# Optimization experiments

Measured on AMD Instinct MI355X. Metric: run time of the kernel, lower is better.

The kernel has to match this reference:

```python
import jax, jax.numpy as jnp
import numpy as np
import math

B, T, D, H = 64, 512, 512, 512


def setup_inputs() -> dict:
    key = jax.random.key(0)
    ks = jax.random.split(key, 32)
    stdv = 1.0 / math.sqrt(H)  # matches reset_parameters()
    u = lambda k, shape: jax.random.uniform(k, shape, jnp.float32, -stdv, stdv)
    inp = {
        "x": jax.random.normal(ks[0], (B, T, D), jnp.float32),
        "h0": jax.random.normal(ks[1], (B, H), jnp.float32),
        "ctx": jax.random.normal(ks[2], (B, T, H), jnp.float32),
    }
    # 9 Linear layers (torch convention: y = x @ W.T + b), weights AND biases uniform(-stdv, stdv)
    names_shapes = [
        ("W_ir", (H, D)), ("b_ir", (H,)), ("W_hr", (H, H)), ("b_hr", (H,)), ("W_pr", (H, H)), ("b_pr", (H,)),
        ("W_ii", (H, D)), ("b_ii", (H,)), ("W_hi", (H, H)), ("b_hi", (H,)), ("W_pi", (H, H)), ("b_pi", (H,)),
        ("W_in", (H, D)), ("b_in", (H,)), ("W_hn", (H, H)), ("b_hn", (H,)), ("W_pn", (H, H)), ("b_pn", (H,)),
    ]
    for i, (nm, sh) in enumerate(names_shapes):
        inp[nm] = u(ks[3 + i], sh)
    return inp


def _forward(x, h0, ctx, W_ir, b_ir, W_hr, b_hr, W_pr, b_pr,
             W_ii, b_ii, W_hi, b_hi, W_pi, b_pi,
             W_in, b_in, W_hn, b_hn, W_pn, b_pn):
    # Precompute all hidden-independent projections for every step: [T,B,H]
    xr = jnp.einsum('btd,hd->tbh', x, W_ir) + b_ir
    xi = jnp.einsum('btd,hd->tbh', x, W_ii) + b_ii
    xn = jnp.einsum('btd,hd->tbh', x, W_in) + b_in
    pr = jnp.einsum('bte,he->tbh', ctx, W_pr) + b_pr
    pi = jnp.einsum('bte,he->tbh', ctx, W_pi) + b_pi
    pn = jnp.einsum('bte,he->tbh', ctx, W_pn) + b_pn

    def step(h, inputs_t):
        xr_t, xi_t, xn_t, pr_t, pi_t, pn_t = inputs_t
        r = jax.nn.sigmoid(xr_t + h @ W_hr.T + b_hr + pr_t)
        i = jax.nn.sigmoid(xi_t + h @ W_hi.T + b_hi + pi_t)
        n = jnp.tanh(xn_t + (r * h) @ W_hn.T + b_hn + pn_t)
        hy = (1.0 - i) * h + i * n
        return hy, hy

    hT, ys = jax.lax.scan(step, h0, (xr, xi, xn, pr, pi, pn))
    return ys.transpose(1, 0, 2), hT  # output [B,T,H], final hidden [B,H]


def reference(x, h0, ctx, W_ir, b_ir, W_hr, b_hr, W_pr, b_pr,
              W_ii, b_ii, W_hi, b_hi, W_pi, b_pi,
              W_in, b_in, W_hn, b_hn, W_pn, b_pn):
    return _forward(x, h0, ctx, W_ir, b_ir, W_hr, b_hr, W_pr, b_pr,
                    W_ii, b_ii, W_hi, b_hi, W_pi, b_pi,
                    W_in, b_in, W_hn, b_hn, W_pn, b_pn)
```

## Files before the change

kernel.cpp:

```cpp
#include <hip/hip_runtime.h>
#include <hip/hip_bf16.h>

typedef __attribute__((ext_vector_type(8))) short short8;
typedef __attribute__((ext_vector_type(4))) float floatx4;

#define TBH ((size_t)16777216)

__device__ __forceinline__ float bfbits2f(unsigned short b) {
  return __uint_as_float(((unsigned int)b) << 16);
}
__device__ __forceinline__ unsigned short f2bf(float f) {
  unsigned int u = __float_as_uint(f);
  unsigned int r = (u + 0x7fffu + ((u >> 16) & 1u)) >> 16;
  return (unsigned short)r;
}

__device__ __forceinline__ void dev_store(unsigned int* p, unsigned int v) {
  __hip_atomic_store(p, v, __ATOMIC_RELAXED, __HIP_MEMORY_SCOPE_AGENT);
}
__device__ __forceinline__ unsigned int dev_load(const unsigned int* p) {
  return __hip_atomic_load(p, __ATOMIC_RELAXED, __HIP_MEMORY_SCOPE_AGENT);
}

#define LBAR()                                              \
  do {                                                      \
    asm volatile("s_waitcnt lgkmcnt(0)" ::: "memory");      \
    __builtin_amdgcn_s_barrier();                           \
    __builtin_amdgcn_sched_barrier(0);                      \
  } while (0)

__global__ void prep_kernel(const float* __restrict__ h0,
                            unsigned int* __restrict__ hpub,
                            unsigned int* __restrict__ rhpub,
                            const float* __restrict__ Whr,
                            const float* __restrict__ Whi,
                            const float* __restrict__ Whn,
                            unsigned short* __restrict__ Whb) {
  int i = blockIdx.x * 256 + threadIdx.x;
  if (i < 64 * 512) {
    hpub[i] = ((unsigned int)f2bf(h0[i])) << 16;
    rhpub[i] = 0u;
  }
#pragma unroll
  for (int rep = 0; rep < 3; ++rep) {
    int j = i + rep * 262144;
    float v = (j < 262144) ? Whr[j] : ((j < 524288) ? Whi[j - 262144] : Whn[j - 524288]);
    Whb[j] = f2bf(v);
  }
}

struct PreArgs {
  const float* x;
  const float* ctx;
  const float* Wi[3];
  const float* Wp[3];
  const float* bi[3];
  const float* bh[3];
  const float* bp[3];
  unsigned short* G;
};

__global__ __launch_bounds__(256) void gemm_pre(PreArgs args) {
  __shared__ short8 a_sm[512];
  __shared__ short8 b_sm[512];
  const int tid = threadIdx.x;
  const int gate = blockIdx.z;
  const int n0 = blockIdx.x * 128;
  const int m0 = blockIdx.y * 128;
  const int wave = tid >> 6, lane = tid & 63;
  const int wm = (wave & 1) * 64, wn = (wave >> 1) * 64;
  const int lm = lane & 15, lq = lane >> 4;
  const float* Wi = args.Wi[gate];
  const float* Wp = args.Wp[gate];

  floatx4 acc[4][4];
#pragma unroll
  for (int i = 0; i < 4; ++i)
#pragma unroll
    for (int j = 0; j < 4; ++j) acc[i][j] = floatx4{0.f, 0.f, 0.f, 0.f};

  for (int kb = 0; kb < 32; ++kb) {
    const float* asrc = (kb < 16) ? args.x : args.ctx;
    const float* bsrc = (kb < 16) ? Wi : Wp;
    const int k0 = (kb & 15) * 32;
    __syncthreads();
#pragma unroll
    for (int c = 0; c < 2; ++c) {
      int s = c * 256 + tid;
      int row = s >> 2, sub = s & 3;
      const float* ap = asrc + (size_t)(m0 + row) * 512 + k0 + sub * 8;
      const float* bp = bsrc + (size_t)(n0 + row) * 512 + k0 + sub * 8;
      float4 a0 = *(const float4*)ap, a1 = *(const float4*)(ap + 4);
      float4 b0 = *(const float4*)bp, b1 = *(const float4*)(bp + 4);
      short8 av, bv;
      av[0] = (short)f2bf(a0.x); av[1] = (short)f2bf(a0.y);
      av[2] = (short)f2bf(a0.z); av[3] = (short)f2bf(a0.w);
      av[4] = (short)f2bf(a1.x); av[5] = (short)f2bf(a1.y);
      av[6] = (short)f2bf(a1.z); av[7] = (short)f2bf(a1.w);
      bv[0] = (short)f2bf(b0.x); bv[1] = (short)f2bf(b0.y);
      bv[2] = (short)f2bf(b0.z); bv[3] = (short)f2bf(b0.w);
      bv[4] = (short)f2bf(b1.x); bv[5] = (short)f2bf(b1.y);
      bv[6] = (short)f2bf(b1.z); bv[7] = (short)f2bf(b1.w);
      a_sm[row * 4 + sub] = av;
      b_sm[row * 4 + sub] = bv;
    }
    __syncthreads();
    short8 af[4], bf[4];
#pragma unroll
    for (int i = 0; i < 4; ++i) af[i] = a_sm[(wm + i * 16 + lm) * 4 + lq];
#pragma unroll
    for (int j = 0; j < 4; ++j) bf[j] = b_sm[(wn + j * 16 + lm) * 4 + lq];
#pragma unroll
    for (int i = 0; i < 4; ++i)
#pragma unroll
      for (int j = 0; j < 4; ++j)
        acc[i][j] = __builtin_amdgcn_mfma_f32_16x16x32_bf16(af[i], bf[j], acc[i][j], 0, 0, 0);
  }

#pragma unroll
  for (int j = 0; j < 4; ++j) {
    int n = n0 + wn + j * 16 + lm;
    float bias = args.bi[gate][n] + args.bh[gate][n] + args.bp[gate][n];
#pragma unroll
    for (int i = 0; i < 4; ++i) {
      int mbase = m0 + wm + i * 16 + lq * 4;
#pragma unroll
      for (int r = 0; r < 4; ++r) {
        int m = mbase + r;
        int t = m & 511, b = m >> 9;
        args.G[(size_t)gate * TBH + (size_t)(t * 64 + b) * 512 + n] = f2bf(acc[i][j][r] + bias);
      }
    }
  }
}

__global__ __launch_bounds__(512, 2) void recur_kernel(
    const unsigned short* __restrict__ G,
    const unsigned short* __restrict__ Whb,
    const float* __restrict__ h0,
    unsigned int* __restrict__ hpub,
    unsigned int* __restrict__ rhpub,
    float* __restrict__ ys,
    float* __restrict__ hT) {
  __shared__ short8 fragbuf[1024];

  const int tid = threadIdx.x;
  const int g = blockIdx.x >> 2;
  const int cb = blockIdx.x & 3;
  const int b0 = g * 16;
  const int c0 = cb * 128;
  const int wave = tid >> 6, lane = tid & 63;
  const int lm = lane & 15, lq = lane >> 4;
  const int cw0 = c0 + wave * 16;
  const int prow = lq * 4;

  short8 wrl[4], wil[4], wnl[4];
  short8 wrr[12], wir[12], wnr[12];
  {
    const unsigned short* Wb = Whb + (size_t)(cw0 + lm) * 512 + lq * 8;
#pragma unroll
    for (int q = 0; q < 4; ++q) {
      const int kb = cb * 4 + q;
      wrl[q] = *(const short8*)(Wb + 0 * 262144 + kb * 32);
      wil[q] = *(const short8*)(Wb + 1 * 262144 + kb * 32);
      wnl[q] = *(const short8*)(Wb + 2 * 262144 + kb * 32);
    }
#pragma unroll
    for (int j = 0; j < 12; ++j) {
      const int kb = (((cb + 1 + (j >> 2)) & 3) << 2) + (j & 3);
      wrr[j] = *(const short8*)(Wb + 0 * 262144 + kb * 32);
      wir[j] = *(const short8*)(Wb + 1 * 262144 + kb * 32);
      wnr[j] = *(const short8*)(Wb + 2 * 262144 + kb * 32);
    }
  }

  const int srow = tid >> 5;
  const int skk = (tid * 4) & 127;
  const int sl = srow + 16 * ((skk >> 3) & 3);
  const int su2 = ((skk >> 5) * 64 + sl) * 2 + ((skk >> 2) & 1);
  uint2* f2 = (uint2*)fragbuf;
  unsigned short* fus = (unsigned short*)fragbuf;

  const int kcol = cw0 + lm;
  const int eidx = ((kcol >> 5) * 64 + 16 * ((kcol >> 3) & 3)) * 8 + (kcol & 7);

  float hreg[4], ireg[4];
#pragma unroll
  for (int r = 0; r < 4; ++r) hreg[r] = h0[(size_t)(b0 + prow + r) * 512 + kcol];
  {
    const float* hp = h0 + (size_t)(b0 + srow) * 512 + c0 + skk;
    float4 v = *(const float4*)hp;
    uint2 p;
    p.x = (unsigned int)f2bf(v.x) | ((unsigned int)f2bf(v.y) << 16);
    p.y = (unsigned int)f2bf(v.z) | ((unsigned int)f2bf(v.w) << 16);
    f2[su2 + cb * 512] = p;
  }
  __syncthreads();

  for (int t = 0; t < 512; ++t) {
    const unsigned int tgh = (unsigned int)t;
    const unsigned int tgr = (unsigned int)(t + 1);

    float gr[4], gi[4];
    const unsigned short* Gt = G + ((size_t)(t * 64 + b0 + prow)) * 512 + kcol;
#pragma unroll
    for (int r = 0; r < 4; ++r) {
      gr[r] = bfbits2f(Gt[r * 512]);
      gi[r] = bfbits2f(Gt[TBH + r * 512]);
    }

    floatx4 ar = {0.f, 0.f, 0.f, 0.f}, ai = {0.f, 0.f, 0.f, 0.f};
    {
      unsigned int v[12];
      unsigned int* hb = hpub + (unsigned)(b0 + srow) * 512;
#pragma unroll
      for (int s = 0; s < 3; ++s) {
        const int off = (((cb + 1 + s) & 3) << 7) + skk;
#pragma unroll
        for (int j = 0; j < 4; ++j) v[s * 4 + j] = dev_load(hb + off + j);
      }
#pragma unroll
      for (int q = 0; q < 4; ++q) {
        short8 hf = fragbuf[(cb * 4 + q) * 64 + lane];
        ar = __builtin_amdgcn_mfma_f32_16x16x32_bf16(hf, wrl[q], ar, 0, 0, 0);
        ai = __builtin_amdgcn_mfma_f32_16x16x32_bf16(hf, wil[q], ai, 0, 0, 0);
      }
      for (;;) {
        bool ok = true;
#pragma unroll
        for (int i = 0; i < 12; ++i) ok &= ((v[i] & 0xffffu) == tgh);
        if (ok) break;
#pragma unroll
        for (int s = 0; s < 3; ++s) {
          bool st = false;
#pragma unroll
          for (int j = 0; j < 4; ++j) st |= ((v[s * 4 + j] & 0xffffu) != tgh);
          if (st) {
            const int off = (((cb + 1 + s) & 3) << 7) + skk;
#pragma unroll
            for (int j = 0; j < 4; ++j) v[s * 4 + j] = dev_load(hb + off + j);
          }
        }
      }
#pragma unroll
      for (int s = 0; s < 3; ++s) {
        const int rcb = (cb + 1 + s) & 3;
        uint2 p;
        p.x = (v[s * 4 + 0] >> 16) | (v[s * 4 + 1] & 0xffff0000u);
        p.y = (v[s * 4 + 2] >> 16) | (v[s * 4 + 3] & 0xffff0000u);
        f2[su2 + rcb * 512] = p;
      }
    }
    LBAR();

#pragma unroll
    for (int j = 0; j < 12; ++j) {
      const int kb = (((cb + 1 + (j >> 2)) & 3) << 2) + (j & 3);
      short8 hf = fragbuf[kb * 64 + lane];
      ar = __builtin_amdgcn_mfma_f32_16x16x32_bf16(hf, wrr[j], ar, 0, 0, 0);
      ai = __builtin_amdgcn_mfma_f32_16x16x32_bf16(hf, wir[j], ai, 0, 0, 0);
    }

    {
      unsigned int* rb = rhpub + (unsigned)(b0 + prow) * 512 + kcol;
#pragma unroll
      for (int r = 0; r < 4; ++r) {
        float sv = 1.f / (1.f + __expf(-(ar[r] + gr[r])));
        float rh = sv * hreg[r];
        ireg[r] = 1.f / (1.f + __expf(-(ai[r] + gi[r])));
        unsigned short rbits = f2bf(rh);
        dev_store(rb + r * 512, (((unsigned int)rbits) << 16) | tgr);
        fus[eidx + (prow + r) * 8] = rbits;
      }
    }
    LBAR();

    float gn[4];
#pragma unroll
    for (int r = 0; r < 4; ++r) gn[r] = bfbits2f(Gt[2 * TBH + r * 512]);

    floatx4 an = {0.f, 0.f, 0.f, 0.f};
    {
      unsigned int v[12];
      unsigned int* rbb = rhpub + (unsigned)(b0 + srow) * 512;
#pragma unroll
      for (int s = 0; s < 3; ++s) {
        const int off = (((cb + 1 + s) & 3) << 7) + skk;
#pragma unroll
        for (int j = 0; j < 4; ++j) v[s * 4 + j] = dev_load(rbb + off + j);
      }
#pragma unroll
      for (int q = 0; q < 4; ++q) {
        short8 hf = fragbuf[(cb * 4 + q) * 64 + lane];
        an = __builtin_amdgcn_mfma_f32_16x16x32_bf16(hf, wnl[q], an, 0, 0, 0);
      }
      for (;;) {
        bool ok = true;
#pragma unroll
        for (int i = 0; i < 12; ++i) ok &= ((v[i] & 0xffffu) == tgr);
        if (ok) break;
#pragma unroll
        for (int s = 0; s < 3; ++s) {
          bool st = false;
#pragma unroll
          for (int j = 0; j < 4; ++j) st |= ((v[s * 4 + j] & 0xffffu) != tgr);
          if (st) {
            const int off = (((cb + 1 + s) & 3) << 7) + skk;
#pragma unroll
            for (int j = 0; j < 4; ++j) v[s * 4 + j] = dev_load(rbb + off + j);
          }
        }
      }
#pragma unroll
      for (int s = 0; s < 3; ++s) {
        const int rcb = (cb + 1 + s) & 3;
        uint2 p;
        p.x = (v[s * 4 + 0] >> 16) | (v[s * 4 + 1] & 0xffff0000u);
        p.y = (v[s * 4 + 2] >> 16) | (v[s * 4 + 3] & 0xffff0000u);
        f2[su2 + rcb * 512] = p;
      }
    }
    LBAR();

#pragma unroll
    for (int j = 0; j < 12; ++j) {
      const int kb = (((cb + 1 + (j >> 2)) & 3) << 2) + (j & 3);
      short8 hf = fragbuf[kb * 64 + lane];
      an = __builtin_amdgcn_mfma_f32_16x16x32_bf16(hf, wnr[j], an, 0, 0, 0);
    }

    {
      unsigned int* hb = hpub + (unsigned)(b0 + prow) * 512 + kcol;
      float* yp = ys + (size_t)(b0 + prow) * 262144 + (size_t)t * 512 + kcol;
#pragma unroll
      for (int r = 0; r < 4; ++r) {
        float pre = an[r] + gn[r];
        float e = __expf(2.f * pre);
        float nv = 1.f - 2.f / (e + 1.f);
        float hy = (1.f - ireg[r]) * hreg[r] + ireg[r] * nv;
        hreg[r] = hy;
        unsigned short hbits = f2bf(hy);
        dev_store(hb + r * 512, (((unsigned int)hbits) << 16) | tgr);
        yp[(size_t)r * 262144] = hy;
        fus[eidx + (prow + r) * 8] = hbits;
      }
      if (t == 511) {
#pragma unroll
        for (int r = 0; r < 4; ++r) hT[(size_t)(b0 + prow + r) * 512 + kcol] = hreg[r];
      }
    }
    LBAR();
  }
}

extern "C" void kernel_launch(void* const* d_in, const int* in_sizes, int n_in,
                              void* d_out, int out_size, void* d_ws, size_t ws_size,
                              hipStream_t stream) {
  typedef const float* cfp;
  cfp x = (cfp)d_in[0];
  cfp h0 = (cfp)d_in[1];
  cfp ctx = (cfp)d_in[2];

  PreArgs pa;
  pa.x = x;
  pa.ctx = ctx;
  for (int gi = 0; gi < 3; ++gi) {
    pa.Wi[gi] = (cfp)d_in[3 + 6 * gi];
    pa.bi[gi] = (cfp)d_in[4 + 6 * gi];
    pa.bh[gi] = (cfp)d_in[6 + 6 * gi];
    pa.Wp[gi] = (cfp)d_in[7 + 6 * gi];
    pa.bp[gi] = (cfp)d_in[8 + 6 * gi];
  }
  cfp Whr = (cfp)d_in[5], Whi = (cfp)d_in[11], Whn = (cfp)d_in[17];

  char* ws = (char*)d_ws;
  unsigned short* G = (unsigned short*)ws;
  size_t off = (size_t)3 * TBH * 2;
  unsigned short* Whb = (unsigned short*)(ws + off);
  off += (size_t)3 * 262144 * 2;
  unsigned int* hpub = (unsigned int*)(ws + off);
  off += (size_t)64 * 512 * 4;
  unsigned int* rhpub = (unsigned int*)(ws + off);
  off += (size_t)64 * 512 * 4;
  pa.G = G;

  float* out = (float*)d_out;
  float* ys = out;
  float* hT = out + (size_t)64 * 512 * 512;

  prep_kernel<<<1024, 256, 0, stream>>>(h0, hpub, rhpub, Whr, Whi, Whn, Whb);
  dim3 gp(4, 256, 3);
  gemm_pre<<<gp, 256, 0, stream>>>(pa);
  recur_kernel<<<16, 512, 0, stream>>>(G, Whb, h0, hpub, rhpub, ys, hT);
}
```

Baseline: 4.173 ms.

## Replace r*h grid sync with partial-sum exchange of r-gate products

The recurrent kernel drops the second cross-block handshake, which published r*h. Each block now computes partial r-gate products over its own K slice for all 64 output columns of its wave and publishes them through a tagged, double-buffered buffer. Peers then reduce those partial sums locally, so r*h for the local columns is built in LDS without a second full h-exchange round. The i-gate weights move to LDS and the n-gate weights stay in registers, G loads are prefetched one step ahead, and h publication is double-buffered. In exchange each step loads and stores more global data (48 partial-sum loads per thread), and the float partial sums lose their low two mantissa bits to the tag.

```diff
diff --git a/kernel.cpp b/kernel.cpp
--- a/kernel.cpp
+++ b/kernel.cpp
@@ -31,7 +31,7 @@
 
 __global__ void prep_kernel(const float* __restrict__ h0,
                             unsigned int* __restrict__ hpub,
-                            unsigned int* __restrict__ rhpub,
+                            unsigned int* __restrict__ PrB,
                             const float* __restrict__ Whr,
                             const float* __restrict__ Whi,
                             const float* __restrict__ Whn,
@@ -39,8 +39,9 @@
   int i = blockIdx.x * 256 + threadIdx.x;
   if (i < 64 * 512) {
     hpub[i] = ((unsigned int)f2bf(h0[i])) << 16;
-    rhpub[i] = 0u;
-  }
+    hpub[32768 + i] = 0x8000u;
+  }
+  PrB[i] = 0u;
 #pragma unroll
   for (int rep = 0; rep < 3; ++rep) {
     int j = i + rep * 262144;
@@ -139,10 +140,11 @@
     const unsigned short* __restrict__ Whb,
     const float* __restrict__ h0,
     unsigned int* __restrict__ hpub,
-    unsigned int* __restrict__ rhpub,
+    unsigned int* __restrict__ PrB,
     float* __restrict__ ys,
     float* __restrict__ hT) {
   __shared__ short8 fragbuf[1024];
+  __shared__ short8 iwsm[8192];
 
   const int tid = threadIdx.x;
   const int g = blockIdx.x >> 2;
@@ -151,28 +153,26 @@
   const int c0 = cb * 128;
   const int wave = tid >> 6, lane = tid & 63;
   const int lm = lane & 15, lq = lane >> 4;
-  const int cw0 = c0 + wave * 16;
+  const int w64 = wave * 64;
+  const int kcol = c0 + wave * 16 + lm;
   const int prow = lq * 4;
 
-  short8 wrl[4], wil[4], wnl[4];
-  short8 wrr[12], wir[12], wnr[12];
-  {
-    const unsigned short* Wb = Whb + (size_t)(cw0 + lm) * 512 + lq * 8;
-#pragma unroll
-    for (int q = 0; q < 4; ++q) {
-      const int kb = cb * 4 + q;
-      wrl[q] = *(const short8*)(Wb + 0 * 262144 + kb * 32);
-      wil[q] = *(const short8*)(Wb + 1 * 262144 + kb * 32);
-      wnl[q] = *(const short8*)(Wb + 2 * 262144 + kb * 32);
-    }
-#pragma unroll
-    for (int j = 0; j < 12; ++j) {
-      const int kb = (((cb + 1 + (j >> 2)) & 3) << 2) + (j & 3);
-      wrr[j] = *(const short8*)(Wb + 0 * 262144 + kb * 32);
-      wir[j] = *(const short8*)(Wb + 1 * 262144 + kb * 32);
-      wnr[j] = *(const short8*)(Wb + 2 * 262144 + kb * 32);
-    }
-  }
+  for (int s = tid; s < 8192; s += 512) {
+    int wv = s >> 10, kb = (s >> 6) & 15, l = s & 63;
+    iwsm[s] = *(const short8*)(Whb + 262144 +
+        (size_t)(c0 + (wv << 4) + (l & 15)) * 512 + kb * 32 + (l >> 4) * 8);
+  }
+  short8 wpr[4][4], wnw[16];
+#pragma unroll
+  for (int n = 0; n < 4; ++n)
+#pragma unroll
+    for (int q = 0; q < 4; ++q)
+      wpr[n][q] = *(const short8*)(Whb +
+          (size_t)(w64 + n * 16 + lm) * 512 + (cb * 4 + q) * 32 + lq * 8);
+#pragma unroll
+  for (int kb = 0; kb < 16; ++kb)
+    wnw[kb] = *(const short8*)(Whb + 2 * 262144 +
+        (size_t)kcol * 512 + kb * 32 + lq * 8);
 
   const int srow = tid >> 5;
   const int skk = (tid * 4) & 127;
@@ -181,174 +181,186 @@
   uint2* f2 = (uint2*)fragbuf;
   unsigned short* fus = (unsigned short*)fragbuf;
 
-  const int kcol = cw0 + lm;
-  const int eidx = ((kcol >> 5) * 64 + 16 * ((kcol >> 3) & 3)) * 8 + (kcol & 7);
-
-  float hreg[4], ireg[4];
-#pragma unroll
-  for (int r = 0; r < 4; ++r) hreg[r] = h0[(size_t)(b0 + prow + r) * 512 + kcol];
-  {
-    const float* hp = h0 + (size_t)(b0 + srow) * 512 + c0 + skk;
-    float4 v = *(const float4*)hp;
-    uint2 p;
-    p.x = (unsigned int)f2bf(v.x) | ((unsigned int)f2bf(v.y) << 16);
-    p.y = (unsigned int)f2bf(v.z) | ((unsigned int)f2bf(v.w) << 16);
-    f2[su2 + cb * 512] = p;
-  }
+  int pub[4], ppos[16], pfix[16];
+#pragma unroll
+  for (int r = 0; r < 4; ++r) pub[r] = (b0 + prow + r) * 512 + kcol;
+#pragma unroll
+  for (int n = 0; n < 4; ++n)
+#pragma unroll
+    for (int r = 0; r < 4; ++r) {
+      int col = w64 + n * 16 + lm;
+      ppos[n * 4 + r] = (prow + r) * 512 + col;
+      pfix[n * 4 + r] = (col >> 5) * 512 + ((col >> 3) & 3) * 128 + (col & 7) + (prow + r) * 8;
+    }
+  const int ecol = (kcol >> 5) * 512 + ((kcol >> 3) & 3) * 128 + (kcol & 7);
+  const int groff = b0 * 512;
+
+  float hreg[4];
+#pragma unroll
+  for (int r = 0; r < 4; ++r) hreg[r] = h0[pub[r]];
+#pragma unroll
+  for (int r = 0; r < 4; ++r) fus[ecol + (prow + r) * 8] = f2bf(hreg[r]);
   __syncthreads();
 
+  unsigned short grc[16], gic[4], gnc[4];
+#pragma unroll
+  for (int k = 0; k < 16; ++k) grc[k] = G[(size_t)(groff + ppos[k])];
+#pragma unroll
+  for (int r = 0; r < 4; ++r) {
+    gic[r] = G[TBH + (size_t)pub[r]];
+    gnc[r] = G[2 * TBH + (size_t)pub[r]];
+  }
+
   for (int t = 0; t < 512; ++t) {
-    const unsigned int tgh = (unsigned int)t;
-    const unsigned int tgr = (unsigned int)(t + 1);
-
-    float gr[4], gi[4];
-    const unsigned short* Gt = G + ((size_t)(t * 64 + b0 + prow)) * 512 + kcol;
-#pragma unroll
-    for (int r = 0; r < 4; ++r) {
-      gr[r] = bfbits2f(Gt[r * 512]);
-      gi[r] = bfbits2f(Gt[TBH + r * 512]);
-    }
-
-    floatx4 ar = {0.f, 0.f, 0.f, 0.f}, ai = {0.f, 0.f, 0.f, 0.f};
-    {
-      unsigned int v[12];
-      unsigned int* hb = hpub + (unsigned)(b0 + srow) * 512;
+    const unsigned int htag = (unsigned int)t;
+    const unsigned int prtag = (unsigned int)((t + 1) & 3);
+    const unsigned int* hsrc = hpub + (t & 1) * 32768;
+    unsigned int* prdst = PrB + (size_t)(t & 1) * 131072 + g * 32768 + cb * 8192;
+    const unsigned int* prsrc = PrB + (size_t)(t & 1) * 131072 + g * 32768;
+
+    floatx4 pr[4];
+#pragma unroll
+    for (int n = 0; n < 4; ++n) pr[n] = floatx4{0.f, 0.f, 0.f, 0.f};
+    short8 hfq[4];
+#pragma unroll
+    for (int q = 0; q < 4; ++q) hfq[q] = fragbuf[(cb * 4 + q) * 64 + lane];
+#pragma unroll
+    for (int n = 0; n < 4; ++n)
+#pragma unroll
+      for (int q = 0; q < 4; ++q)
+        pr[n] = __builtin_amdgcn_mfma_f32_16x16x32_bf16(hfq[q], wpr[n][q], pr[n], 0, 0, 0);
+#pragma unroll
+    for (int n = 0; n < 4; ++n)
+#pragma unroll
+      for (int r = 0; r < 4; ++r)
+        dev_store((unsigned int*)prdst + ppos[n * 4 + r],
+                  (__float_as_uint(pr[n][r]) & 0xFFFFFFFCu) | prtag);
+
+    unsigned int hv[12];
+    const unsigned int* hb = hsrc + (unsigned)(b0 + srow) * 512;
+#pragma unroll
+    for (int s = 0; s < 3; ++s) {
+      const int off = (((cb + 1 + s) & 3) << 7) + skk;
+#pragma unroll
+      for (int j = 0; j < 4; ++j) hv[s * 4 + j] = dev_load(hb + off + j);
+    }
+    unsigned int pv[48];
+#pragma unroll
+    for (int s = 0; s < 3; ++s) {
+      const int sb = ((cb + 1 + s) & 3) * 8192;
+#pragma unroll
+      for (int k = 0; k < 16; ++k) pv[s * 16 + k] = dev_load(prsrc + sb + ppos[k]);
+    }
+
+    for (;;) {
+      bool ok = true;
+#pragma unroll
+      for (int i = 0; i < 12; ++i) ok &= ((hv[i] & 0xffffu) == htag);
+      if (ok) break;
 #pragma unroll
       for (int s = 0; s < 3; ++s) {
-        const int off = (((cb + 1 + s) & 3) << 7) + skk;
-#pragma unroll
-        for (int j = 0; j < 4; ++j) v[s * 4 + j] = dev_load(hb + off + j);
-      }
-#pragma unroll
-      for (int q = 0; q < 4; ++q) {
-        short8 hf = fragbuf[(cb * 4 + q) * 64 + lane];
-        ar = __builtin_amdgcn_mfma_f32_16x16x32_bf16(hf, wrl[q], ar, 0, 0, 0);
-        ai = __builtin_amdgcn_mfma_f32_16x16x32_bf16(hf, wil[q], ai, 0, 0, 0);
-      }
-      for (;;) {
-        bool ok = true;
-#pragma unroll
-        for (int i = 0; i < 12; ++i) ok &= ((v[i] & 0xffffu) == tgh);
-        if (ok) break;
-#pragma unroll
-        for (int s = 0; s < 3; ++s) {
-          bool st = false;
-#pragma unroll
-          for (int j = 0; j < 4; ++j) st |= ((v[s * 4 + j] & 0xffffu) != tgh);
-          if (st) {
-            const int off = (((cb + 1 + s) & 3) << 7) + skk;
-#pragma unroll
-            for (int j = 0; j < 4; ++j) v[s * 4 + j] = dev_load(hb + off + j);
-          }
+        bool st = false;
+#pragma unroll
+        for (int j = 0; j < 4; ++j) st |= ((hv[s * 4 + j] & 0xffffu) != htag);
+        if (st) {
+          const int off = (((cb + 1 + s) & 3) << 7) + skk;
+#pragma unroll
+          for (int j = 0; j < 4; ++j) hv[s * 4 + j] = dev_load(hb + off + j);
         }
       }
+    }
+#pragma unroll
+    for (int s = 0; s < 3; ++s) {
+      const int rcb = (cb + 1 + s) & 3;
+      uint2 p;
+      p.x = (hv[s * 4 + 0] >> 16) | (hv[s * 4 + 1] & 0xffff0000u);
+      p.y = (hv[s * 4 + 2] >> 16) | (hv[s * 4 + 3] & 0xffff0000u);
+      f2[su2 + rcb * 512] = p;
+    }
+    LBAR();
+
+    floatx4 ia = {0.f, 0.f, 0.f, 0.f};
+#pragma unroll
+    for (int kb = 0; kb < 16; ++kb)
+      ia = __builtin_amdgcn_mfma_f32_16x16x32_bf16(
+          fragbuf[kb * 64 + lane], iwsm[(wave * 16 + kb) * 64 + lane], ia, 0, 0, 0);
+
+    for (;;) {
+      bool ok = true;
+#pragma unroll
+      for (int i = 0; i < 48; ++i) ok &= ((pv[i] & 3u) == prtag);
+      if (ok) break;
 #pragma unroll
       for (int s = 0; s < 3; ++s) {
-        const int rcb = (cb + 1 + s) & 3;
-        uint2 p;
-        p.x = (v[s * 4 + 0] >> 16) | (v[s * 4 + 1] & 0xffff0000u);
-        p.y = (v[s * 4 + 2] >> 16) | (v[s * 4 + 3] & 0xffff0000u);
-        f2[su2 + rcb * 512] = p;
-      }
-    }
-    LBAR();
-
-#pragma unroll
-    for (int j = 0; j < 12; ++j) {
-      const int kb = (((cb + 1 + (j >> 2)) & 3) << 2) + (j & 3);
-      short8 hf = fragbuf[kb * 64 + lane];
-      ar = __builtin_amdgcn_mfma_f32_16x16x32_bf16(hf, wrr[j], ar, 0, 0, 0);
-      ai = __builtin_amdgcn_mfma_f32_16x16x32_bf16(hf, wir[j], ai, 0, 0, 0);
-    }
-
-    {
-      unsigned int* rb = rhpub + (unsigned)(b0 + prow) * 512 + kcol;
-#pragma unroll
-      for (int r = 0; r < 4; ++r) {
-        float sv = 1.f / (1.f + __expf(-(ar[r] + gr[r])));
-        float rh = sv * hreg[r];
-        ireg[r] = 1.f / (1.f + __expf(-(ai[r] + gi[r])));
-        unsigned short rbits = f2bf(rh);
-        dev_store(rb + r * 512, (((unsigned int)rbits) << 16) | tgr);
-        fus[eidx + (prow + r) * 8] = rbits;
-      }
-    }
-    LBAR();
-
-    float gn[4];
-#pragma unroll
-    for (int r = 0; r < 4; ++r) gn[r] = bfbits2f(Gt[2 * TBH + r * 512]);
-
-    floatx4 an = {0.f, 0.f, 0.f, 0.f};
-    {
-      unsigned int v[12];
-      unsigned int* rbb = rhpub + (unsigned)(b0 + srow) * 512;
-#pragma unroll
-      for (int s = 0; s < 3; ++s) {
-        const int off = (((cb + 1 + s) & 3) << 7) + skk;
-#pragma unroll
-        for (int j = 0; j < 4; ++j) v[s * 4 + j] = dev_load(rbb + off + j);
-      }
-#pragma unroll
-      for (int q = 0; q < 4; ++q) {
-        short8 hf = fragbuf[(cb * 4 + q) * 64 + lane];
-        an = __builtin_amdgcn_mfma_f32_16x16x32_bf16(hf, wnl[q], an, 0, 0, 0);
-      }
-      for (;;) {
-        bool ok = true;
-#pragma unroll
-        for (int i = 0; i < 12; ++i) ok &= ((v[i] & 0xffffu) == tgr);
-        if (ok) break;
-#pragma unroll
-        for (int s = 0; s < 3; ++s) {
-          bool st = false;
-#pragma unroll
-          for (int j = 0; j < 4; ++j) st |= ((v[s * 4 + j] & 0xffffu) != tgr);
-          if (st) {
-            const int off = (((cb + 1 + s) & 3) << 7) + skk;
-#pragma unroll
-            for (int j = 0; j < 4; ++j) v[s * 4 + j] = dev_load(rbb + off + j);
-          }
+        bool st = false;
+#pragma unroll
+        for (int k = 0; k < 16; ++k) st |= ((pv[s * 16 + k] & 3u) != prtag);
+        if (st) {
+          const int sb = ((cb + 1 + s) & 3) * 8192;
+#pragma unroll
+          for (int k = 0; k < 16; ++k) pv[s * 16 + k] = dev_load(prsrc + sb + ppos[k]);
         }
       }
-#pragma unroll
-      for (int s = 0; s < 3; ++s) {
-        const int rcb = (cb + 1 + s) & 3;
-        uint2 p;
-        p.x = (v[s * 4 + 0] >> 16) | (v[s * 4 + 1] & 0xffff0000u);
-        p.y = (v[s * 4 + 2] >> 16) | (v[s * 4 + 3] & 0xffff0000u);
-        f2[su2 + rcb * 512] = p;
-      }
-    }
+    }
+
+    unsigned short rhb[16];
+#pragma unroll
+    for (int k = 0; k < 16; ++k) {
+      int n = k >> 2, r = k & 3;
+      float rsum = pr[n][r] + bfbits2f(grc[k]) +
+                   __uint_as_float(pv[k] & 0xFFFFFFFCu) +
+                   __uint_as_float(pv[16 + k] & 0xFFFFFFFCu) +
+                   __uint_as_float(pv[32 + k] & 0xFFFFFFFCu);
+      float rv = 1.f / (1.f + __expf(-rsum));
+      rhb[k] = f2bf(rv * bfbits2f(fus[pfix[k]]));
+    }
+    float ireg[4];
+#pragma unroll
+    for (int r = 0; r < 4; ++r) ireg[r] = 1.f / (1.f + __expf(-(ia[r] + bfbits2f(gic[r]))));
     LBAR();
 
 #pragma unroll
-    for (int j = 0; j < 12; ++j) {
-      const int kb = (((cb + 1 + (j >> 2)) & 3) << 2) + (j & 3);
-      short8 hf = fragbuf[kb * 64 + lane];
-      an = __builtin_amdgcn_mfma_f32_16x16x32_bf16(hf, wnr[j], an, 0, 0, 0);
-    }
-
-    {
-      unsigned int* hb = hpub + (unsigned)(b0 + prow) * 512 + kcol;
-      float* yp = ys + (size_t)(b0 + prow) * 262144 + (size_t)t * 512 + kcol;
-#pragma unroll
-      for (int r = 0; r < 4; ++r) {
-        float pre = an[r] + gn[r];
-        float e = __expf(2.f * pre);
-        float nv = 1.f - 2.f / (e + 1.f);
-        float hy = (1.f - ireg[r]) * hreg[r] + ireg[r] * nv;
-        hreg[r] = hy;
-        unsigned short hbits = f2bf(hy);
-        dev_store(hb + r * 512, (((unsigned int)hbits) << 16) | tgr);
-        yp[(size_t)r * 262144] = hy;
-        fus[eidx + (prow + r) * 8] = hbits;
-      }
-      if (t == 511) {
-#pragma unroll
-        for (int r = 0; r < 4; ++r) hT[(size_t)(b0 + prow + r) * 512 + kcol] = hreg[r];
-      }
-    }
+    for (int k = 0; k < 16; ++k) fus[pfix[k]] = rhb[k];
+    LBAR();
+
+    floatx4 na = {0.f, 0.f, 0.f, 0.f};
+#pragma unroll
+    for (int kb = 0; kb < 16; ++kb)
+      na = __builtin_amdgcn_mfma_f32_16x16x32_bf16(
+          fragbuf[kb * 64 + lane], wnw[kb], na, 0, 0, 0);
+
+    const int tp = (t + 1 < 512) ? t + 1 : 511;
+    unsigned short grn[16], gin[4], gnn[4];
+#pragma unroll
+    for (int k = 0; k < 16; ++k) grn[k] = G[(size_t)tp * 32768 + groff + ppos[k]];
+#pragma unroll
+    for (int r = 0; r < 4; ++r) {
+      gin[r] = G[TBH + (size_t)tp * 32768 + pub[r]];
+      gnn[r] = G[2 * TBH + (size_t)tp * 32768 + pub[r]];
+    }
+    LBAR();
+
+    unsigned int* hdst = hpub + ((t + 1) & 1) * 32768;
+#pragma unroll
+    for (int r = 0; r < 4; ++r) {
+      float pre = na[r] + bfbits2f(gnc[r]);
+      float e = __expf(2.f * pre);
+      float nv = 1.f - 2.f / (e + 1.f);
+      float hy = (1.f - ireg[r]) * hreg[r] + ireg[r] * nv;
+      hreg[r] = hy;
+      unsigned short hbits = f2bf(hy);
+      dev_store(hdst + pub[r], (((unsigned int)hbits) << 16) | (unsigned int)(t + 1));
+      fus[ecol + (prow + r) * 8] = hbits;
+      ys[(size_t)(b0 + prow + r) * 262144 + (size_t)t * 512 + kcol] = hy;
+    }
+    if (t == 511) {
+#pragma unroll
+      for (int r = 0; r < 4; ++r) hT[pub[r]] = hreg[r];
+    }
+#pragma unroll
+    for (int k = 0; k < 16; ++k) grc[k] = grn[k];
+#pragma unroll
+    for (int r = 0; r < 4; ++r) { gic[r] = gin[r]; gnc[r] = gnn[r]; }
     LBAR();
   }
 }
@@ -379,17 +391,17 @@
   unsigned short* Whb = (unsigned short*)(ws + off);
   off += (size_t)3 * 262144 * 2;
   unsigned int* hpub = (unsigned int*)(ws + off);
-  off += (size_t)64 * 512 * 4;
-  unsigned int* rhpub = (unsigned int*)(ws + off);
-  off += (size_t)64 * 512 * 4;
+  off += (size_t)2 * 64 * 512 * 4;
+  unsigned int* PrB = (unsigned int*)(ws + off);
+  off += (size_t)2 * 4 * 4 * 16 * 512 * 4;
   pa.G = G;
 
   float* out = (float*)d_out;
   float* ys = out;
   float* hT = out + (size_t)64 * 512 * 512;
 
-  prep_kernel<<<1024, 256, 0, stream>>>(h0, hpub, rhpub, Whr, Whi, Whn, Whb);
+  prep_kernel<<<1024, 256, 0, stream>>>(h0, hpub, PrB, Whr, Whi, Whn, Whb);
   dim3 gp(4, 256, 3);
   gemm_pre<<<gp, 256, 0, stream>>>(pa);
-  recur_kernel<<<16, 512, 0, stream>>>(G, Whb, h0, hpub, rhpub, ys, hT);
-}
+  recur_kernel<<<16, 512, 0, stream>>>(G, Whb, h0, hpub, PrB, ys, hT);
+}
```

Result: slower. 10.76 ms (+157.8%).

## Split recurrence across 32 blocks with XCD-local fast sync path

Applied to the files above, without the earlier changes.

Launches 32 recurrent blocks instead of 16, each covering 8 batch rows instead of 16, so per-step work is spread over more CUs. At startup the blocks check whether all four column-partners share the same XCD and pass a ping test. If they do, the exchange uses L2-coherent sc0 vector loads and volatile stores instead of agent-scope atomics. It also prefetches the next step's G values and uses dwordx4 polling loads. The risk is that half the lanes idle (only lq<2 is active) and that the fast path relies on an XCD co-location assumption, which falls back to the slow path when it does not hold.

```diff
diff --git a/kernel.cpp b/kernel.cpp
--- a/kernel.cpp
+++ b/kernel.cpp
@@ -3,6 +3,7 @@
 
 typedef __attribute__((ext_vector_type(8))) short short8;
 typedef __attribute__((ext_vector_type(4))) float floatx4;
+typedef __attribute__((ext_vector_type(4))) unsigned int uintx4;
 
 #define TBH ((size_t)16777216)
 
@@ -20,6 +21,50 @@
 }
 __device__ __forceinline__ unsigned int dev_load(const unsigned int* p) {
   return __hip_atomic_load(p, __ATOMIC_RELAXED, __HIP_MEMORY_SCOPE_AGENT);
+}
+
+template <bool FAST>
+__device__ __forceinline__ void exst(unsigned int* p, unsigned int v) {
+  if constexpr (FAST) {
+    *(volatile unsigned int*)p = v;
+  } else {
+    dev_store(p, v);
+  }
+}
+
+template <bool FAST>
+__device__ __forceinline__ uintx4 exld4(const unsigned int* p) {
+  uintx4 r;
+  if constexpr (FAST) {
+    asm volatile("global_load_dwordx4 %0, %1, off sc0\n\ts_waitcnt vmcnt(0)"
+                 : "=&v"(r) : "v"(p) : "memory");
+  } else {
+    r[0] = dev_load(p); r[1] = dev_load(p + 1);
+    r[2] = dev_load(p + 2); r[3] = dev_load(p + 3);
+  }
+  return r;
+}
+
+template <bool FAST>
+__device__ __forceinline__ void exld4x3(const unsigned int* p0, const unsigned int* p1,
+                                        const unsigned int* p2,
+                                        uintx4& a, uintx4& b, uintx4& c) {
+  if constexpr (FAST) {
+    asm volatile(
+        "global_load_dwordx4 %0, %3, off sc0\n\t"
+        "global_load_dwordx4 %1, %4, off sc0\n\t"
+        "global_load_dwordx4 %2, %5, off sc0\n\t"
+        "s_waitcnt vmcnt(0)"
+        : "=&v"(a), "=&v"(b), "=&v"(c)
+        : "v"(p0), "v"(p1), "v"(p2) : "memory");
+  } else {
+    a = exld4<false>(p0); b = exld4<false>(p1); c = exld4<false>(p2);
+  }
+}
+
+__device__ __forceinline__ bool tagok(uintx4 v, unsigned int tag) {
+  return ((v[0] & 0xffffu) == tag) & ((v[1] & 0xffffu) == tag) &
+         ((v[2] & 0xffffu) == tag) & ((v[3] & 0xffffu) == tag);
 }
 
 #define LBAR()                                              \
@@ -32,6 +77,7 @@
 __global__ void prep_kernel(const float* __restrict__ h0,
                             unsigned int* __restrict__ hpub,
                             unsigned int* __restrict__ rhpub,
+                            unsigned int* __restrict__ aux,
                             const float* __restrict__ Whr,
                             const float* __restrict__ Whi,
                             const float* __restrict__ Whn,
@@ -41,6 +87,7 @@
     hpub[i] = ((unsigned int)f2bf(h0[i])) << 16;
     rhpub[i] = 0u;
   }
+  if (i < 576) aux[i] = 0u;
 #pragma unroll
   for (int rep = 0; rep < 3; ++rep) {
     int j = i + rep * 262144;
@@ -134,223 +181,272 @@
   }
 }
 
+template <bool FAST>
+__device__ __forceinline__ void recur_body(
+    const unsigned short* __restrict__ G,
+    const unsigned short* __restrict__ Whb,
+    const float* __restrict__ h0,
+    unsigned int* __restrict__ hpub,
+    unsigned int* __restrict__ rhpub,
+    float* __restrict__ ys,
+    float* __restrict__ hT,
+    short8* fragbuf) {
+  const int tid = threadIdx.x;
+  const int bid = blockIdx.x;
+  const int c = bid & 7;
+  const int cb = bid >> 3;
+  const int b0 = c * 8;
+  const int c0 = cb * 128;
+  const int wave = tid >> 6, lane = tid & 63;
+  const int lm = lane & 15, lq = lane >> 4;
+  const int kcol = c0 + wave * 16 + lm;
+  const int prow = lq * 4;
+  const bool pv = (lq < 2);
+
+  const unsigned short* Wb = Whb + (size_t)kcol * 512 + lq * 8;
+  short8 wrl[4], wil[4], wnl[4], wrr[12], wir[12], wnr[12];
+#pragma unroll
+  for (int q = 0; q < 4; ++q) {
+    const int kb = cb * 4 + q;
+    wrl[q] = *(const short8*)(Wb + 0 * 262144 + kb * 32);
+    wil[q] = *(const short8*)(Wb + 1 * 262144 + kb * 32);
+    wnl[q] = *(const short8*)(Wb + 2 * 262144 + kb * 32);
+  }
+#pragma unroll
+  for (int j = 0; j < 12; ++j) {
+    const int kb = (((cb + 1 + (j >> 2)) & 3) << 2) + (j & 3);
+    wrr[j] = *(const short8*)(Wb + 0 * 262144 + kb * 32);
+    wir[j] = *(const short8*)(Wb + 1 * 262144 + kb * 32);
+    wnr[j] = *(const short8*)(Wb + 2 * 262144 + kb * 32);
+  }
+
+  const int srow = tid >> 5;
+  const int skk = (tid * 4) & 127;
+  const int sl = srow + 16 * ((skk >> 3) & 3);
+  const int su2 = ((skk >> 5) * 64 + sl) * 2 + ((skk >> 2) & 1);
+  const int rcb0 = (cb + 1) & 3, rcb1 = (cb + 2) & 3, rcb2 = (cb + 3) & 3;
+  const int roff0 = (b0 + srow) * 512 + rcb0 * 128 + skk;
+  const int roff1 = (b0 + srow) * 512 + rcb1 * 128 + skk;
+  const int roff2 = (b0 + srow) * 512 + rcb2 * 128 + skk;
+  uint2* f2 = (uint2*)fragbuf;
+  unsigned short* fus = (unsigned short*)fragbuf;
+  const int ecol = (kcol >> 5) * 512 + ((kcol >> 3) & 3) * 128 + (kcol & 7);
+
+  int pub[4];
+#pragma unroll
+  for (int r = 0; r < 4; ++r) pub[r] = (b0 + prow + r) * 512 + kcol;
+
+#pragma unroll
+  for (int k = 0; k < 4; ++k) f2[tid + 512 * k] = uint2{0u, 0u};
+  __syncthreads();
+
+  float hreg[4] = {0.f, 0.f, 0.f, 0.f}, ireg[4];
+  unsigned short grc[4], gic[4], gnc[4];
+  if (pv) {
+#pragma unroll
+    for (int r = 0; r < 4; ++r) {
+      hreg[r] = h0[pub[r]];
+      fus[ecol + (prow + r) * 8] = f2bf(hreg[r]);
+    }
+    const unsigned short* Gt = G + (size_t)(b0 + prow) * 512 + kcol;
+#pragma unroll
+    for (int r = 0; r < 4; ++r) {
+      grc[r] = Gt[r * 512];
+      gic[r] = Gt[TBH + r * 512];
+      gnc[r] = Gt[2 * TBH + r * 512];
+    }
+  }
+  __syncthreads();
+
+  for (int t = 0; t < 512; ++t) {
+    const unsigned int htag = (unsigned int)t;
+    const unsigned int rtag = (unsigned int)(t + 1);
+
+    uintx4 hv0, hv1, hv2;
+    if (tid < 256) exld4x3<FAST>(hpub + roff0, hpub + roff1, hpub + roff2, hv0, hv1, hv2);
+    floatx4 ar = {0.f, 0.f, 0.f, 0.f}, ai = {0.f, 0.f, 0.f, 0.f};
+    short8 hfq[4];
+#pragma unroll
+    for (int q = 0; q < 4; ++q) hfq[q] = fragbuf[(cb * 4 + q) * 64 + lane];
+#pragma unroll
+    for (int q = 0; q < 4; ++q) {
+      ar = __builtin_amdgcn_mfma_f32_16x16x32_bf16(hfq[q], wrl[q], ar, 0, 0, 0);
+      ai = __builtin_amdgcn_mfma_f32_16x16x32_bf16(hfq[q], wil[q], ai, 0, 0, 0);
+    }
+    if (tid < 256) {
+      for (;;) {
+        bool o0 = tagok(hv0, htag), o1 = tagok(hv1, htag), o2 = tagok(hv2, htag);
+        if (o0 & o1 & o2) break;
+        if (!o0) hv0 = exld4<FAST>(hpub + roff0);
+        if (!o1) hv1 = exld4<FAST>(hpub + roff1);
+        if (!o2) hv2 = exld4<FAST>(hpub + roff2);
+      }
+      uint2 p;
+      p.x = (hv0[0] >> 16) | (hv0[1] & 0xffff0000u);
+      p.y = (hv0[2] >> 16) | (hv0[3] & 0xffff0000u);
+      f2[su2 + rcb0 * 512] = p;
+      p.x = (hv1[0] >> 16) | (hv1[1] & 0xffff0000u);
+      p.y = (hv1[2] >> 16) | (hv1[3] & 0xffff0000u);
+      f2[su2 + rcb1 * 512] = p;
+      p.x = (hv2[0] >> 16) | (hv2[1] & 0xffff0000u);
+      p.y = (hv2[2] >> 16) | (hv2[3] & 0xffff0000u);
+      f2[su2 + rcb2 * 512] = p;
+    }
+    const int tp = (t + 1 < 512) ? t + 1 : 511;
+    unsigned short grn[4], gin[4], gnn[4];
+    if (pv) {
+      const unsigned short* Gt1 = G + (size_t)(tp * 64 + b0 + prow) * 512 + kcol;
+#pragma unroll
+      for (int r = 0; r < 4; ++r) {
+        grn[r] = Gt1[r * 512];
+        gin[r] = Gt1[TBH + r * 512];
+        gnn[r] = Gt1[2 * TBH + r * 512];
+      }
+    }
+    LBAR();
+
+#pragma unroll
+    for (int j = 0; j < 12; ++j) {
+      const int kb = (((cb + 1 + (j >> 2)) & 3) << 2) + (j & 3);
+      short8 hf = fragbuf[kb * 64 + lane];
+      ar = __builtin_amdgcn_mfma_f32_16x16x32_bf16(hf, wrr[j], ar, 0, 0, 0);
+      ai = __builtin_amdgcn_mfma_f32_16x16x32_bf16(hf, wir[j], ai, 0, 0, 0);
+    }
+    unsigned short rhb[4];
+    if (pv) {
+#pragma unroll
+      for (int r = 0; r < 4; ++r) {
+        float sv = 1.f / (1.f + __expf(-(ar[r] + bfbits2f(grc[r]))));
+        ireg[r] = 1.f / (1.f + __expf(-(ai[r] + bfbits2f(gic[r]))));
+        rhb[r] = f2bf(sv * hreg[r]);
+        exst<FAST>(rhpub + pub[r], (((unsigned int)rhb[r]) << 16) | rtag);
+      }
+    }
+    LBAR();
+    if (pv) {
+#pragma unroll
+      for (int r = 0; r < 4; ++r) fus[ecol + (prow + r) * 8] = rhb[r];
+    }
+    LBAR();
+
+    uintx4 rv0, rv1, rv2;
+    if (tid < 256) exld4x3<FAST>(rhpub + roff0, rhpub + roff1, rhpub + roff2, rv0, rv1, rv2);
+    floatx4 an = {0.f, 0.f, 0.f, 0.f};
+#pragma unroll
+    for (int q = 0; q < 4; ++q)
+      an = __builtin_amdgcn_mfma_f32_16x16x32_bf16(
+          fragbuf[(cb * 4 + q) * 64 + lane], wnl[q], an, 0, 0, 0);
+    if (tid < 256) {
+      for (;;) {
+        bool o0 = tagok(rv0, rtag), o1 = tagok(rv1, rtag), o2 = tagok(rv2, rtag);
+        if (o0 & o1 & o2) break;
+        if (!o0) rv0 = exld4<FAST>(rhpub + roff0);
+        if (!o1) rv1 = exld4<FAST>(rhpub + roff1);
+        if (!o2) rv2 = exld4<FAST>(rhpub + roff2);
+      }
+      uint2 p;
+      p.x = (rv0[0] >> 16) | (rv0[1] & 0xffff0000u);
+      p.y = (rv0[2] >> 16) | (rv0[3] & 0xffff0000u);
+      f2[su2 + rcb0 * 512] = p;
+      p.x = (rv1[0] >> 16) | (rv1[1] & 0xffff0000u);
+      p.y = (rv1[2] >> 16) | (rv1[3] & 0xffff0000u);
+      f2[su2 + rcb1 * 512] = p;
+      p.x = (rv2[0] >> 16) | (rv2[1] & 0xffff0000u);
+      p.y = (rv2[2] >> 16) | (rv2[3] & 0xffff0000u);
+      f2[su2 + rcb2 * 512] = p;
+    }
+    LBAR();
+
+#pragma unroll
+    for (int j = 0; j < 12; ++j) {
+      const int kb = (((cb + 1 + (j >> 2)) & 3) << 2) + (j & 3);
+      an = __builtin_amdgcn_mfma_f32_16x16x32_bf16(
+          fragbuf[kb * 64 + lane], wnr[j], an, 0, 0, 0);
+    }
+    LBAR();
+
+    if (pv) {
+#pragma unroll
+      for (int r = 0; r < 4; ++r) {
+        float pre = an[r] + bfbits2f(gnc[r]);
+        float e = __expf(2.f * pre);
+        float nv = 1.f - 2.f / (e + 1.f);
+        float hy = (1.f - ireg[r]) * hreg[r] + ireg[r] * nv;
+        hreg[r] = hy;
+        unsigned short hb = f2bf(hy);
+        exst<FAST>(hpub + pub[r], (((unsigned int)hb) << 16) | rtag);
+        fus[ecol + (prow + r) * 8] = hb;
+        ys[(size_t)(b0 + prow + r) * 262144 + (size_t)t * 512 + kcol] = hy;
+      }
+      if (t == 511) {
+#pragma unroll
+        for (int r = 0; r < 4; ++r) hT[pub[r]] = hreg[r];
+      }
+#pragma unroll
+      for (int r = 0; r < 4; ++r) { grc[r] = grn[r]; gic[r] = gin[r]; gnc[r] = gnn[r]; }
+    }
+    LBAR();
+  }
+}
+
 __global__ __launch_bounds__(512, 2) void recur_kernel(
     const unsigned short* __restrict__ G,
     const unsigned short* __restrict__ Whb,
     const float* __restrict__ h0,
     unsigned int* __restrict__ hpub,
     unsigned int* __restrict__ rhpub,
+    unsigned int* __restrict__ aux,
     float* __restrict__ ys,
     float* __restrict__ hT) {
   __shared__ short8 fragbuf[1024];
-
-  const int tid = threadIdx.x;
-  const int g = blockIdx.x >> 2;
-  const int cb = blockIdx.x & 3;
-  const int b0 = g * 16;
-  const int c0 = cb * 128;
-  const int wave = tid >> 6, lane = tid & 63;
-  const int lm = lane & 15, lq = lane >> 4;
-  const int cw0 = c0 + wave * 16;
-  const int prow = lq * 4;
-
-  short8 wrl[4], wil[4], wnl[4];
-  short8 wrr[12], wir[12], wnr[12];
-  {
-    const unsigned short* Wb = Whb + (size_t)(cw0 + lm) * 512 + lq * 8;
-#pragma unroll
-    for (int q = 0; q < 4; ++q) {
-      const int kb = cb * 4 + q;
-      wrl[q] = *(const short8*)(Wb + 0 * 262144 + kb * 32);
-      wil[q] = *(const short8*)(Wb + 1 * 262144 + kb * 32);
-      wnl[q] = *(const short8*)(Wb + 2 * 262144 + kb * 32);
-    }
-#pragma unroll
-    for (int j = 0; j < 12; ++j) {
-      const int kb = (((cb + 1 + (j >> 2)) & 3) << 2) + (j & 3);
-      wrr[j] = *(const short8*)(Wb + 0 * 262144 + kb * 32);
-      wir[j] = *(const short8*)(Wb + 1 * 262144 + kb * 32);
-      wnr[j] = *(const short8*)(Wb + 2 * 262144 + kb * 32);
-    }
-  }
-
-  const int srow = tid >> 5;
-  const int skk = (tid * 4) & 127;
-  const int sl = srow + 16 * ((skk >> 3) & 3);
-  const int su2 = ((skk >> 5) * 64 + sl) * 2 + ((skk >> 2) & 1);
-  uint2* f2 = (uint2*)fragbuf;
-  unsigned short* fus = (unsigned short*)fragbuf;
-
-  const int kcol = cw0 + lm;
-  const int eidx = ((kcol >> 5) * 64 + 16 * ((kcol >> 3) & 3)) * 8 + (kcol & 7);
-
-  float hreg[4], ireg[4];
-#pragma unroll
-  for (int r = 0; r < 4; ++r) hreg[r] = h0[(size_t)(b0 + prow + r) * 512 + kcol];
-  {
-    const float* hp = h0 + (size_t)(b0 + srow) * 512 + c0 + skk;
-    float4 v = *(const float4*)hp;
-    uint2 p;
-    p.x = (unsigned int)f2bf(v.x) | ((unsigned int)f2bf(v.y) << 16);
-    p.y = (unsigned int)f2bf(v.z) | ((unsigned int)f2bf(v.w) << 16);
-    f2[su2 + cb * 512] = p;
-  }
-  __syncthreads();
-
-  for (int t = 0; t < 512; ++t) {
-    const unsigned int tgh = (unsigned int)t;
-    const unsigned int tgr = (unsigned int)(t + 1);
-
-    float gr[4], gi[4];
-    const unsigned short* Gt = G + ((size_t)(t * 64 + b0 + prow)) * 512 + kcol;
-#pragma unroll
-    for (int r = 0; r < 4; ++r) {
-      gr[r] = bfbits2f(Gt[r * 512]);
-      gi[r] = bfbits2f(Gt[TBH + r * 512]);
-    }
-
-    floatx4 ar = {0.f, 0.f, 0.f, 0.f}, ai = {0.f, 0.f, 0.f, 0.f};
-    {
-      unsigned int v[12];
-      unsigned int* hb = hpub + (unsigned)(b0 + srow) * 512;
-#pragma unroll
-      for (int s = 0; s < 3; ++s) {
-        const int off = (((cb + 1 + s) & 3) << 7) + skk;
-#pragma unroll
-        for (int j = 0; j < 4; ++j) v[s * 4 + j] = dev_load(hb + off + j);
-      }
-#pragma unroll
-      for (int q = 0; q < 4; ++q) {
-        short8 hf = fragbuf[(cb * 4 + q) * 64 + lane];
-        ar = __builtin_amdgcn_mfma_f32_16x16x32_bf16(hf, wrl[q], ar, 0, 0, 0);
-        ai = __builtin_amdgcn_mfma_f32_16x16x32_bf16(hf, wil[q], ai, 0, 0, 0);
-      }
-      for (;;) {
-        bool ok = true;
-#pragma unroll
-        for (int i = 0; i < 12; ++i) ok &= ((v[i] & 0xffffu) == tgh);
-        if (ok) break;
-#pragma unroll
-        for (int s = 0; s < 3; ++s) {
-          bool st = false;
-#pragma unroll
-          for (int j = 0; j < 4; ++j) st |= ((v[s * 4 + j] & 0xffffu) != tgh);
-          if (st) {
-            const int off = (((cb + 1 + s) & 3) << 7) + skk;
-#pragma unroll
-            for (int j = 0; j < 4; ++j) v[s * 4 + j] = dev_load(hb + off + j);
+  __shared__ int fastsh;
+  const int bid = blockIdx.x;
+
+  if (threadIdx.x == 0) {
+    unsigned int* xcdb = aux;
+    unsigned int* pingb = aux + 32;
+    unsigned int* verd = aux + 544;
+    unsigned int myx;
+    asm volatile("s_getreg_b32 %0, hwreg(HW_REG_XCC_ID)" : "=s"(myx));
+    dev_store(&xcdb[bid], (myx & 0xffu) | 0x100u);
+    unsigned int xs[4];
+    for (int s = 0; s < 4; ++s) {
+      unsigned int q;
+      do { q = dev_load(&xcdb[(bid & 7) + (s << 3)]); } while (q < 0x100u);
+      xs[s] = q;
+    }
+    unsigned int okv = (xs[0] == xs[1]) & (xs[1] == xs[2]) & (xs[2] == xs[3]);
+    if (okv) {
+      int budget = 40000;
+      for (int round = 1; round <= 8 && okv; ++round) {
+        *(volatile unsigned int*)&pingb[bid * 16] = (unsigned int)round;
+        for (int s = 0; s < 4 && okv; ++s) {
+          const unsigned int* pp = &pingb[((bid & 7) + (s << 3)) * 16];
+          unsigned int q;
+          for (;;) {
+            asm volatile("global_load_dword %0, %1, off sc0\n\ts_waitcnt vmcnt(0)"
+                         : "=&v"(q) : "v"(pp) : "memory");
+            if (q >= (unsigned int)round) break;
+            if (--budget <= 0) { okv = 0u; break; }
           }
         }
       }
-#pragma unroll
-      for (int s = 0; s < 3; ++s) {
-        const int rcb = (cb + 1 + s) & 3;
-        uint2 p;
-        p.x = (v[s * 4 + 0] >> 16) | (v[s * 4 + 1] & 0xffff0000u);
-        p.y = (v[s * 4 + 2] >> 16) | (v[s * 4 + 3] & 0xffff0000u);
-        f2[su2 + rcb * 512] = p;
-      }
-    }
-    LBAR();
-
-#pragma unroll
-    for (int j = 0; j < 12; ++j) {
-      const int kb = (((cb + 1 + (j >> 2)) & 3) << 2) + (j & 3);
-      short8 hf = fragbuf[kb * 64 + lane];
-      ar = __builtin_amdgcn_mfma_f32_16x16x32_bf16(hf, wrr[j], ar, 0, 0, 0);
-      ai = __builtin_amdgcn_mfma_f32_16x16x32_bf16(hf, wir[j], ai, 0, 0, 0);
-    }
-
-    {
-      unsigned int* rb = rhpub + (unsigned)(b0 + prow) * 512 + kcol;
-#pragma unroll
-      for (int r = 0; r < 4; ++r) {
-        float sv = 1.f / (1.f + __expf(-(ar[r] + gr[r])));
-        float rh = sv * hreg[r];
-        ireg[r] = 1.f / (1.f + __expf(-(ai[r] + gi[r])));
-        unsigned short rbits = f2bf(rh);
-        dev_store(rb + r * 512, (((unsigned int)rbits) << 16) | tgr);
-        fus[eidx + (prow + r) * 8] = rbits;
-      }
-    }
-    LBAR();
-
-    float gn[4];
-#pragma unroll
-    for (int r = 0; r < 4; ++r) gn[r] = bfbits2f(Gt[2 * TBH + r * 512]);
-
-    floatx4 an = {0.f, 0.f, 0.f, 0.f};
-    {
-      unsigned int v[12];
-      unsigned int* rbb = rhpub + (unsigned)(b0 + srow) * 512;
-#pragma unroll
-      for (int s = 0; s < 3; ++s) {
-        const int off = (((cb + 1 + s) & 3) << 7) + skk;
-#pragma unroll
-        for (int j = 0; j < 4; ++j) v[s * 4 + j] = dev_load(rbb + off + j);
-      }
-#pragma unroll
-      for (int q = 0; q < 4; ++q) {
-        short8 hf = fragbuf[(cb * 4 + q) * 64 + lane];
-        an = __builtin_amdgcn_mfma_f32_16x16x32_bf16(hf, wnl[q], an, 0, 0, 0);
-      }
-      for (;;) {
-        bool ok = true;
-#pragma unroll
-        for (int i = 0; i < 12; ++i) ok &= ((v[i] & 0xffffu) == tgr);
-        if (ok) break;
-#pragma unroll
-        for (int s = 0; s < 3; ++s) {
-          bool st = false;
-#pragma unroll
-          for (int j = 0; j < 4; ++j) st |= ((v[s * 4 + j] & 0xffffu) != tgr);
-          if (st) {
-            const int off = (((cb + 1 + s) & 3) << 7) + skk;
-#pragma unroll
-            for (int j = 0; j < 4; ++j) v[s * 4 + j] = dev_load(rbb + off + j);
-          }
-        }
-      }
-#pragma unroll
-      for (int s = 0; s < 3; ++s) {
-        const int rcb = (cb + 1 + s) & 3;
-        uint2 p;
-        p.x = (v[s * 4 + 0] >> 16) | (v[s * 4 + 1] & 0xffff0000u);
-        p.y = (v[s * 4 + 2] >> 16) | (v[s * 4 + 3] & 0xffff0000u);
-        f2[su2 + rcb * 512] = p;
-      }
-    }
-    LBAR();
-
-#pragma unroll
-    for (int j = 0; j < 12; ++j) {
-      const int kb = (((cb + 1 + (j >> 2)) & 3) << 2) + (j & 3);
-      short8 hf = fragbuf[kb * 64 + lane];
-      an = __builtin_amdgcn_mfma_f32_16x16x32_bf16(hf, wnr[j], an, 0, 0, 0);
-    }
-
-    {
-      unsigned int* hb = hpub + (unsigned)(b0 + prow) * 512 + kcol;
-      float* yp = ys + (size_t)(b0 + prow) * 262144 + (size_t)t * 512 + kcol;
-#pragma unroll
-      for (int r = 0; r < 4; ++r) {
-        float pre = an[r] + gn[r];
-        float e = __expf(2.f * pre);
-        float nv = 1.f - 2.f / (e + 1.f);
-        float hy = (1.f - ireg[r]) * hreg[r] + ireg[r] * nv;
-        hreg[r] = hy;
-        unsigned short hbits = f2bf(hy);
-        dev_store(hb + r * 512, (((unsigned int)hbits) << 16) | tgr);
-        yp[(size_t)r * 262144] = hy;
-        fus[eidx + (prow + r) * 8] = hbits;
-      }
-      if (t == 511) {
-#pragma unroll
-        for (int r = 0; r < 4; ++r) hT[(size_t)(b0 + prow + r) * 512 + kcol] = hreg[r];
-      }
-    }
-    LBAR();
-  }
+    }
+    dev_store(&verd[bid], okv | 0x100u);
+    unsigned int allok = 1u;
+    for (int s = 0; s < 4; ++s) {
+      unsigned int q;
+      do { q = dev_load(&verd[(bid & 7) + (s << 3)]); } while (q < 0x100u);
+      allok &= (q & 1u);
+    }
+    fastsh = (int)allok;
+  }
+  __syncthreads();
+
+  if (fastsh)
+    recur_body<true>(G, Whb, h0, hpub, rhpub, ys, hT, fragbuf);
+  else
+    recur_body<false>(G, Whb, h0, hpub, rhpub, ys, hT, fragbuf);
 }
 
 extern "C" void kernel_launch(void* const* d_in, const int* in_sizes, int n_in,
@@ -382,14 +478,16 @@
   off += (size_t)64 * 512 * 4;
   unsigned int* rhpub = (unsigned int*)(ws + off);
   off += (size_t)64 * 512 * 4;
+  unsigned int* aux = (unsigned int*)(ws + off);
+  off += (size_t)576 * 4;
   pa.G = G;
 
   float* out = (float*)d_out;
   float* ys = out;
   float* hT = out + (size_t)64 * 512 * 512;
 
-  prep_kernel<<<1024, 256, 0, stream>>>(h0, hpub, rhpub, Whr, Whi, Whn, Whb);
+  prep_kernel<<<1024, 256, 0, stream>>>(h0, hpub, rhpub, aux, Whr, Whi, Whn, Whb);
   dim3 gp(4, 256, 3);
   gemm_pre<<<gp, 256, 0, stream>>>(pa);
-  recur_kernel<<<16, 512, 0, stream>>>(G, Whb, h0, hpub, rhpub, ys, hT);
-}
+  recur_kernel<<<32, 512, 0, stream>>>(G, Whb, h0, hpub, rhpub, aux, ys, hT);
+}
```

Result: slower. 10.23 ms (+145.2%).
